# Kernel optimization log

Hardware: AMD Instinct MI355X
Metric: run time of the kernel (lower is better)

Reference implementation:

```python
import jax, jax.numpy as jnp
import numpy as np

H = 65  # LSTM units / vocab size
L = 3   # stacked layers (shared weights)

def _lstm_step(x, h, c, W, U, b):
    # Keras LSTMCell gate order: i, f, c(bar), o
    z = x @ W + h @ U + b  # [B, 4H]
    i, f, g, o = jnp.split(z, 4, axis=-1)
    i = jax.nn.sigmoid(i)
    f = jax.nn.sigmoid(f)
    g = jnp.tanh(g)
    o = jax.nn.sigmoid(o)
    c_new = f * c + i * g
    h_new = o * jnp.tanh(c_new)
    return h_new, c_new

def setup_inputs() -> dict:
    key = jax.random.key(0)
    ks = jax.random.split(key, 4)
    B, T = 50, 4096
    x = jax.random.normal(ks[0], (B, T, H), dtype=jnp.float32)
    s = 1.0 / np.sqrt(H)
    W = jax.random.normal(ks[1], (H, 4 * H), dtype=jnp.float32) * s
    U = jax.random.normal(ks[2], (H, 4 * H), dtype=jnp.float32) * s
    b = jnp.zeros((4 * H,), dtype=jnp.float32)
    Wd = jax.random.normal(ks[3], (H, H), dtype=jnp.float32) * s
    bd = jnp.zeros((H,), dtype=jnp.float32)
    return {"x": x, "W": W, "U": U, "b": b, "Wd": Wd, "bd": bd}

def reference(x, W, U, b, Wd, bd):
    B, T, _ = x.shape
    h0 = jnp.zeros((L, B, H), dtype=x.dtype)
    c0 = jnp.zeros((L, B, H), dtype=x.dtype)

    def step(carry, x_t):
        h, c = carry  # each [L, B, H]
        inp = x_t
        hs, cs = [], []
        for l in range(L):  # 3 layers, SAME weights (shared cell object)
            h_l, c_l = _lstm_step(inp, h[l], c[l], W, U, b)
            hs.append(h_l)
            cs.append(c_l)
            inp = h_l
        return (jnp.stack(hs), jnp.stack(cs)), inp  # output = top-layer hidden

    _, ys = jax.lax.scan(step, (h0, c0), jnp.swapaxes(x, 0, 1))  # ys: [T, B, H]
    ys = jnp.swapaxes(ys, 0, 1)  # [B, T, H]
    return ys @ Wd + bd
```

## Files before the change

### kernel.cpp

```cpp
#include <hip/hip_runtime.h>


#define HH    65
#define G4    260
#define TT    4096
#define NB    50
#define BLOCK 1024
#define DROWS 64

using v2f = __attribute__((ext_vector_type(2))) float;
#define PKFMA(a, b, c) __builtin_elementwise_fma((a), (b), (c))
#define KEEP(s) asm volatile("" : "+v"(s))

__device__ __forceinline__ float sigm(float x)  { return 1.0f / (1.0f + __expf(-x)); }
__device__ __forceinline__ float tanha(float x) { float e = __expf(2.0f * x); return 1.0f - 2.0f / (e + 1.0f); }

__device__ __forceinline__ float qsum8(float v) {
    int i = __float_as_int(v);
    v += __int_as_float(__builtin_amdgcn_update_dpp(0, i, 0xB1,  0xF, 0xF, true));
    i = __float_as_int(v);
    v += __int_as_float(__builtin_amdgcn_update_dpp(0, i, 0x4E,  0xF, 0xF, true));
    i = __float_as_int(v);
    v += __int_as_float(__builtin_amdgcn_update_dpp(0, i, 0x141, 0xF, 0xF, true));
    return v;
}

__global__ void __launch_bounds__(BLOCK)
__attribute__((amdgpu_waves_per_eu(4, 4)))
charrnn_rec(const float* __restrict__ x, const float* __restrict__ W,
            const float* __restrict__ U, const float* __restrict__ bv,
            float* __restrict__ out)
{
    __shared__ __align__(16) float s_hin[3][68];
    __shared__ __align__(16) float s_hrec[3][68];
    __shared__ __align__(16) float s_z[3][2][256];
    __shared__ float s_parte[3][2][4];

    const int bat  = blockIdx.x;
    const int tid  = threadIdx.x;
    const int lane = tid & 63;
    const int wv   = tid >> 6;
    const float* xb   = x   + (size_t)bat * TT * HH;
    float*       outb = out + (size_t)bat * TT * HH;

    for (int i = tid; i < 3 * 68; i += BLOCK) { (&s_hin[0][0])[i] = 0.0f; (&s_hrec[0][0])[i] = 0.0f; }

    const int w    = tid & 7;
    const int qC   = (tid >> 3) & 63;
    const int col0 = qC * 4;
    const int side = tid >> 9;
    const float* M = side ? U : W;

    v2f wa0, wa1, wa2, wa3, wb0, wb1, wb2, wb3,
        wc0, wc1, wc2, wc3, wd0, wd1, wd2, wd3;
#define WLD(v, c, q)                                                          \
    do {                                                                      \
        float t0 = M[(8 * w + 2 * (q) + 0) * G4 + col0 + (c)];                \
        float t1 = M[(8 * w + 2 * (q) + 1) * G4 + col0 + (c)];                \
        KEEP(t0); KEEP(t1);                                                   \
        v = (v2f){t0, t1};                                                    \
    } while (0)
    WLD(wa0, 0, 0); WLD(wa1, 0, 1); WLD(wa2, 0, 2); WLD(wa3, 0, 3);
    WLD(wb0, 1, 0); WLD(wb1, 1, 1); WLD(wb2, 1, 2); WLD(wb3, 1, 3);
    WLD(wc0, 2, 0); WLD(wc1, 2, 1); WLD(wc2, 2, 2); WLD(wc3, 2, 3);
    WLD(wd0, 3, 0); WLD(wd1, 3, 1); WLD(wd2, 3, 2); WLD(wd3, 3, 3);
#undef WLD
    float ws0 = (w == 7) ? M[64 * G4 + col0 + 0] : 0.0f; KEEP(ws0);
    float ws1 = (w == 7) ? M[64 * G4 + col0 + 1] : 0.0f; KEEP(ws1);
    float ws2 = (w == 7) ? M[64 * G4 + col0 + 2] : 0.0f; KEEP(ws2);
    float ws3 = (w == 7) ? M[64 * G4 + col0 + 3] : 0.0f; KEEP(ws3);

    const bool isX  = ((wv == 0) || (wv == 9)) && (lane < 32);
    const int  colX = 256 + ((lane >> 3) & 3);
    v2f e0, e1, e2, e3;
#define ELD(v, q)                                                             \
    do {                                                                      \
        float t0 = isX ? M[(8 * w + 2 * (q) + 0) * G4 + colX] : 0.0f;         \
        float t1 = isX ? M[(8 * w + 2 * (q) + 1) * G4 + colX] : 0.0f;         \
        KEEP(t0); KEEP(t1);                                                   \
        v = (v2f){t0, t1};                                                    \
    } while (0)
    ELD(e0, 0); ELD(e1, 1); ELD(e2, 2); ELD(e3, 3);
#undef ELD
    float esc = (isX && w == 7) ? M[64 * G4 + colX] : 0.0f; KEEP(esc);

    const int  cl = tid / 65, n = tid - (tid / 65) * 65;
    const bool isC = (tid < 195);
    const float bz0 = bv[n], bz1 = bv[65 + n], bz2 = bv[130 + n], bz3 = bv[195 + n];
    float creg = 0.0f;

    const bool isP  = (tid >= 959);
    const int  pidx = tid - 959;
    float cur = 0.0f, nxt = 0.0f;
    if (isP) {
        s_hin[0][pidx] = xb[pidx];
        cur = xb[HH + pidx];
    }
    __syncthreads();

    for (int r = 0; r < TT + 2; ++r) {
        if (isP) {
            const int tn = r + 2;
            nxt = (tn < TT) ? xb[(size_t)tn * HH + pidx] : 0.0f;
        }
#pragma unroll
        for (int l = 0; l < 3; ++l) {
            if ((unsigned)(r - l) < TT) {
                const float* hb = side ? &s_hrec[l][0] : &s_hin[l][0];
                const float4* h4 = (const float4*)(hb + 8 * w);
                const float4 H0 = h4[0], H1 = h4[1];
                const float  h64 = hb[64];
                const v2f hA = (v2f){H0.x, H0.y}, hB = (v2f){H0.z, H0.w};
                const v2f hC = (v2f){H1.x, H1.y}, hD = (v2f){H1.z, H1.w};
                float a0, a1, a2, a3;
#define CD(res, p0, p1, p2, p3, ps)                                           \
    {   v2f ac = hA * p0;                                                     \
        ac = PKFMA(hB, p1, ac);                                               \
        ac = PKFMA(hC, p2, ac);                                               \
        ac = PKFMA(hD, p3, ac);                                               \
        res = fmaf(h64, ps, ac.x + ac.y); }
                CD(a0, wa0, wa1, wa2, wa3, ws0)
                CD(a1, wb0, wb1, wb2, wb3, ws1)
                CD(a2, wc0, wc1, wc2, wc3, ws2)
                CD(a3, wd0, wd1, wd2, wd3, ws3)
                a0 = qsum8(a0); a1 = qsum8(a1); a2 = qsum8(a2); a3 = qsum8(a3);
                if ((lane & 7) == 0)
                    *(float4*)&s_z[l][side][col0] = make_float4(a0, a1, a2, a3);
                if (isX) {
                    float ea;
                    CD(ea, e0, e1, e2, e3, esc)
                    ea = qsum8(ea);
                    if ((lane & 7) == 0) s_parte[l][side][(lane >> 3) & 3] = ea;
                }
#undef CD
            }
        }
        __syncthreads();

        if (isC) {
            if ((unsigned)(r - cl) < TT) {
                const float zi = bz0 + s_z[cl][0][n]       + s_z[cl][1][n];
                const float zf = bz1 + s_z[cl][0][65 + n]  + s_z[cl][1][65 + n];
                const float zg = bz2 + s_z[cl][0][130 + n] + s_z[cl][1][130 + n];
                float zo;
                if (n < 61) zo = bz3 + s_z[cl][0][195 + n]    + s_z[cl][1][195 + n];
                else        zo = bz3 + s_parte[cl][0][n - 61] + s_parte[cl][1][n - 61];
                const float ig = sigm(zi), fg = sigm(zf), gg = tanha(zg), og = sigm(zo);
                creg = fmaf(fg, creg, ig * gg);
                const float h = og * tanha(creg);
                s_hrec[cl][n] = h;
                if (cl < 2) s_hin[cl + 1][n] = h;
                else        outb[(size_t)(r - cl) * HH + n] = h;
            }
        }
        if (isP) {
            if (r + 1 < TT) s_hin[0][pidx] = cur;
            cur = nxt;
        }
        __syncthreads();
    }
}

__global__ void __launch_bounds__(256, 1)
dense_head(float* __restrict__ io, const float* __restrict__ Wd, const float* __restrict__ bd)
{
    __shared__ __align__(16) float s_h[DROWS][68];
    __shared__ float s_wd[HH][HH];
    __shared__ float s_bd[HH];

    const int tid = threadIdx.x;
    float* base = io + (size_t)blockIdx.x * DROWS * HH;

    for (int i = tid; i < DROWS * HH; i += 256) {
        const int row = i / HH, k = i - row * HH;
        s_h[row][k] = base[i];
    }
    for (int i = tid; i < HH * HH; i += 256) (&s_wd[0][0])[i] = Wd[i];
    if (tid < HH) s_bd[tid] = bd[tid];
    __syncthreads();

    for (int u = tid; u < DROWS * HH; u += 256) {
        const int row = u / HH, c = u - row * HH;
        const float4* hp = (const float4*)&s_h[row][0];
        float acc = s_bd[c];
#pragma unroll
        for (int k4 = 0; k4 < 16; ++k4) {
            const float4 hv = hp[k4];
            acc = fmaf(hv.x, s_wd[4 * k4 + 0][c], acc);
            acc = fmaf(hv.y, s_wd[4 * k4 + 1][c], acc);
            acc = fmaf(hv.z, s_wd[4 * k4 + 2][c], acc);
            acc = fmaf(hv.w, s_wd[4 * k4 + 3][c], acc);
        }
        acc = fmaf(s_h[row][64], s_wd[64][c], acc);
        base[u] = acc;
    }
}

extern "C" void kernel_launch(void* const* d_in, const int* in_sizes, int n_in,
                              void* d_out, int out_size, void* d_ws, size_t ws_size,
                              hipStream_t stream)
{
    const float* x  = (const float*)d_in[0];
    const float* W  = (const float*)d_in[1];
    const float* U  = (const float*)d_in[2];
    const float* bv = (const float*)d_in[3];
    const float* Wd = (const float*)d_in[4];
    const float* bd = (const float*)d_in[5];
    float* out = (float*)d_out;

    hipLaunchKernelGGL(charrnn_rec, dim3(NB), dim3(BLOCK), 0, stream, x, W, U, bv, out);
    hipLaunchKernelGGL(dense_head, dim3(NB * TT / DROWS), dim3(256), 0, stream, out, Wd, bd);
}
```

Baseline: 6.721 ms.

## Fuse gate reduction and cell update per unit, one barrier per step

Each hidden unit is now owned by 8 lanes (4 covering W, 4 covering U). Each lane holds all four gate columns for that unit, so the DPP reduction directly produces the full gate pre-activations and the cell update runs in-lane. This drops the shared-memory z buffer and the second __syncthreads per step, and uses ping-pong buffers for h and x. In exchange, the block shrinks to 640 threads, each thread keeps twice as many weights in registers, and the activation math is computed redundantly across the 8 lanes.

```diff
diff --git a/kernel.cpp b/kernel.cpp
--- a/kernel.cpp
+++ b/kernel.cpp
@@ -5,7 +5,8 @@
 #define G4    260
 #define TT    4096
 #define NB    50
-#define BLOCK 1024
+#define BLOCK 640
+#define NMAIN 520
 #define DROWS 64
 
 using v2f = __attribute__((ext_vector_type(2))) float;
@@ -26,138 +27,125 @@
 }
 
 __global__ void __launch_bounds__(BLOCK)
-__attribute__((amdgpu_waves_per_eu(4, 4)))
+__attribute__((amdgpu_waves_per_eu(2, 3)))
 charrnn_rec(const float* __restrict__ x, const float* __restrict__ W,
             const float* __restrict__ U, const float* __restrict__ bv,
             float* __restrict__ out)
 {
-    __shared__ __align__(16) float s_hin[3][68];
-    __shared__ __align__(16) float s_hrec[3][68];
-    __shared__ __align__(16) float s_z[3][2][256];
-    __shared__ float s_parte[3][2][4];
-
-    const int bat  = blockIdx.x;
-    const int tid  = threadIdx.x;
-    const int lane = tid & 63;
-    const int wv   = tid >> 6;
+    __shared__ __align__(16) float s_h[3][2][68];
+    __shared__ __align__(16) float s_x[2][68];
+
+    const int bat = blockIdx.x, tid = threadIdx.x;
     const float* xb   = x   + (size_t)bat * TT * HH;
     float*       outb = out + (size_t)bat * TT * HH;
 
-    for (int i = tid; i < 3 * 68; i += BLOCK) { (&s_hin[0][0])[i] = 0.0f; (&s_hrec[0][0])[i] = 0.0f; }
-
-    const int w    = tid & 7;
-    const int qC   = (tid >> 3) & 63;
-    const int col0 = qC * 4;
-    const int side = tid >> 9;
-    const float* M = side ? U : W;
-
-    v2f wa0, wa1, wa2, wa3, wb0, wb1, wb2, wb3,
-        wc0, wc1, wc2, wc3, wd0, wd1, wd2, wd3;
-#define WLD(v, c, q)                                                          \
+    for (int i = tid; i < 3 * 2 * 68; i += BLOCK) (&s_h[0][0][0])[i] = 0.0f;
+
+    const bool isM  = (tid < NMAIN);
+    const int  n    = tid >> 3;
+    const int  j    = tid & 7;
+    const int  side = j >> 2;
+    const int  q    = j & 3;
+    const int  kst  = 16 * q;
+    const float* M  = side ? U : W;
+
+    v2f wA0, wA1, wA2, wA3, wA4, wA5, wA6, wA7,
+        wB0, wB1, wB2, wB3, wB4, wB5, wB6, wB7,
+        wC0, wC1, wC2, wC3, wC4, wC5, wC6, wC7,
+        wD0, wD1, wD2, wD3, wD4, wD5, wD6, wD7;
+#define WLD(v, g, pp)                                                         \
     do {                                                                      \
-        float t0 = M[(8 * w + 2 * (q) + 0) * G4 + col0 + (c)];                \
-        float t1 = M[(8 * w + 2 * (q) + 1) * G4 + col0 + (c)];                \
+        float t0 = isM ? M[(kst + 2 * (pp) + 0) * G4 + n + 65 * (g)] : 0.0f;  \
+        float t1 = isM ? M[(kst + 2 * (pp) + 1) * G4 + n + 65 * (g)] : 0.0f;  \
         KEEP(t0); KEEP(t1);                                                   \
         v = (v2f){t0, t1};                                                    \
     } while (0)
-    WLD(wa0, 0, 0); WLD(wa1, 0, 1); WLD(wa2, 0, 2); WLD(wa3, 0, 3);
-    WLD(wb0, 1, 0); WLD(wb1, 1, 1); WLD(wb2, 1, 2); WLD(wb3, 1, 3);
-    WLD(wc0, 2, 0); WLD(wc1, 2, 1); WLD(wc2, 2, 2); WLD(wc3, 2, 3);
-    WLD(wd0, 3, 0); WLD(wd1, 3, 1); WLD(wd2, 3, 2); WLD(wd3, 3, 3);
+    WLD(wA0, 0, 0); WLD(wA1, 0, 1); WLD(wA2, 0, 2); WLD(wA3, 0, 3);
+    WLD(wA4, 0, 4); WLD(wA5, 0, 5); WLD(wA6, 0, 6); WLD(wA7, 0, 7);
+    WLD(wB0, 1, 0); WLD(wB1, 1, 1); WLD(wB2, 1, 2); WLD(wB3, 1, 3);
+    WLD(wB4, 1, 4); WLD(wB5, 1, 5); WLD(wB6, 1, 6); WLD(wB7, 1, 7);
+    WLD(wC0, 2, 0); WLD(wC1, 2, 1); WLD(wC2, 2, 2); WLD(wC3, 2, 3);
+    WLD(wC4, 2, 4); WLD(wC5, 2, 5); WLD(wC6, 2, 6); WLD(wC7, 2, 7);
+    WLD(wD0, 3, 0); WLD(wD1, 3, 1); WLD(wD2, 3, 2); WLD(wD3, 3, 3);
+    WLD(wD4, 3, 4); WLD(wD5, 3, 5); WLD(wD6, 3, 6); WLD(wD7, 3, 7);
 #undef WLD
-    float ws0 = (w == 7) ? M[64 * G4 + col0 + 0] : 0.0f; KEEP(ws0);
-    float ws1 = (w == 7) ? M[64 * G4 + col0 + 1] : 0.0f; KEEP(ws1);
-    float ws2 = (w == 7) ? M[64 * G4 + col0 + 2] : 0.0f; KEEP(ws2);
-    float ws3 = (w == 7) ? M[64 * G4 + col0 + 3] : 0.0f; KEEP(ws3);
-
-    const bool isX  = ((wv == 0) || (wv == 9)) && (lane < 32);
-    const int  colX = 256 + ((lane >> 3) & 3);
-    v2f e0, e1, e2, e3;
-#define ELD(v, q)                                                             \
-    do {                                                                      \
-        float t0 = isX ? M[(8 * w + 2 * (q) + 0) * G4 + colX] : 0.0f;         \
-        float t1 = isX ? M[(8 * w + 2 * (q) + 1) * G4 + colX] : 0.0f;         \
-        KEEP(t0); KEEP(t1);                                                   \
-        v = (v2f){t0, t1};                                                    \
-    } while (0)
-    ELD(e0, 0); ELD(e1, 1); ELD(e2, 2); ELD(e3, 3);
-#undef ELD
-    float esc = (isX && w == 7) ? M[64 * G4 + colX] : 0.0f; KEEP(esc);
-
-    const int  cl = tid / 65, n = tid - (tid / 65) * 65;
-    const bool isC = (tid < 195);
-    const float bz0 = bv[n], bz1 = bv[65 + n], bz2 = bv[130 + n], bz3 = bv[195 + n];
-    float creg = 0.0f;
-
-    const bool isP  = (tid >= 959);
-    const int  pidx = tid - 959;
+    const bool hasTail = isM && (q == 3);
+    float wsA = hasTail ? M[64 * G4 + n]           : 0.0f; KEEP(wsA);
+    float wsB = hasTail ? M[64 * G4 + n + 65]      : 0.0f; KEEP(wsB);
+    float wsC = hasTail ? M[64 * G4 + n + 130]     : 0.0f; KEEP(wsC);
+    float wsD = hasTail ? M[64 * G4 + n + 195]     : 0.0f; KEEP(wsD);
+
+    const float bz0 = isM ? bv[n]       : 0.0f;
+    const float bz1 = isM ? bv[65 + n]  : 0.0f;
+    const float bz2 = isM ? bv[130 + n] : 0.0f;
+    const float bz3 = isM ? bv[195 + n] : 0.0f;
+
+    const int pidx = (tid >= 576) ? (tid - 576) : ((tid == NMAIN) ? 64 : -1);
     float cur = 0.0f, nxt = 0.0f;
-    if (isP) {
-        s_hin[0][pidx] = xb[pidx];
+    if (pidx >= 0) {
+        s_x[0][pidx] = xb[pidx];
         cur = xb[HH + pidx];
     }
+
+    float creg0 = 0.0f, creg1 = 0.0f, creg2 = 0.0f;
+    int p = 0;
     __syncthreads();
 
     for (int r = 0; r < TT + 2; ++r) {
-        if (isP) {
+        if (pidx >= 0) {
             const int tn = r + 2;
             nxt = (tn < TT) ? xb[(size_t)tn * HH + pidx] : 0.0f;
         }
+        if (isM) {
 #pragma unroll
-        for (int l = 0; l < 3; ++l) {
-            if ((unsigned)(r - l) < TT) {
-                const float* hb = side ? &s_hrec[l][0] : &s_hin[l][0];
-                const float4* h4 = (const float4*)(hb + 8 * w);
-                const float4 H0 = h4[0], H1 = h4[1];
-                const float  h64 = hb[64];
-                const v2f hA = (v2f){H0.x, H0.y}, hB = (v2f){H0.z, H0.w};
-                const v2f hC = (v2f){H1.x, H1.y}, hD = (v2f){H1.z, H1.w};
-                float a0, a1, a2, a3;
-#define CD(res, p0, p1, p2, p3, ps)                                           \
-    {   v2f ac = hA * p0;                                                     \
-        ac = PKFMA(hB, p1, ac);                                               \
-        ac = PKFMA(hC, p2, ac);                                               \
-        ac = PKFMA(hD, p3, ac);                                               \
-        res = fmaf(h64, ps, ac.x + ac.y); }
-                CD(a0, wa0, wa1, wa2, wa3, ws0)
-                CD(a1, wb0, wb1, wb2, wb3, ws1)
-                CD(a2, wc0, wc1, wc2, wc3, ws2)
-                CD(a3, wd0, wd1, wd2, wd3, ws3)
-                a0 = qsum8(a0); a1 = qsum8(a1); a2 = qsum8(a2); a3 = qsum8(a3);
-                if ((lane & 7) == 0)
-                    *(float4*)&s_z[l][side][col0] = make_float4(a0, a1, a2, a3);
-                if (isX) {
-                    float ea;
-                    CD(ea, e0, e1, e2, e3, esc)
-                    ea = qsum8(ea);
-                    if ((lane & 7) == 0) s_parte[l][side][(lane >> 3) & 3] = ea;
+            for (int l = 0; l < 3; ++l) {
+                if ((unsigned)(r - l) < TT) {
+                    const float* hb = side ? &s_h[l][p][0]
+                                           : (l == 0 ? &s_x[p][0] : &s_h[l - 1][p][0]);
+                    const float4* h4 = (const float4*)(hb + kst);
+                    const float4 H0 = h4[0], H1 = h4[1], H2 = h4[2], H3 = h4[3];
+                    const float  h64 = hb[64];
+                    const v2f hA = (v2f){H0.x, H0.y}, hB = (v2f){H0.z, H0.w},
+                              hC = (v2f){H1.x, H1.y}, hD = (v2f){H1.z, H1.w},
+                              hE = (v2f){H2.x, H2.y}, hF = (v2f){H2.z, H2.w},
+                              hG = (v2f){H3.x, H3.y}, hHv = (v2f){H3.z, H3.w};
+                    float a0, a1, a2, a3;
+#define CD(res, P0, P1, P2, P3, P4, P5, P6, P7, S)                            \
+    {   v2f ac = hA * P0;                                                     \
+        ac = PKFMA(hB, P1, ac);  ac = PKFMA(hC, P2, ac);                      \
+        ac = PKFMA(hD, P3, ac);  ac = PKFMA(hE, P4, ac);                      \
+        ac = PKFMA(hF, P5, ac);  ac = PKFMA(hG, P6, ac);                      \
+        ac = PKFMA(hHv, P7, ac);                                              \
+        res = fmaf(h64, S, ac.x + ac.y); }
+                    CD(a0, wA0, wA1, wA2, wA3, wA4, wA5, wA6, wA7, wsA)
+                    CD(a1, wB0, wB1, wB2, wB3, wB4, wB5, wB6, wB7, wsB)
+                    CD(a2, wC0, wC1, wC2, wC3, wC4, wC5, wC6, wC7, wsC)
+                    CD(a3, wD0, wD1, wD2, wD3, wD4, wD5, wD6, wD7, wsD)
+#undef CD
+                    const float z0 = qsum8(a0) + bz0;
+                    const float z1 = qsum8(a1) + bz1;
+                    const float z2 = qsum8(a2) + bz2;
+                    const float z3 = qsum8(a3) + bz3;
+                    const float ig = sigm(z0), fg = sigm(z1),
+                                gg = tanha(z2), og = sigm(z3);
+                    float c;
+                    if (l == 0)      { creg0 = fmaf(fg, creg0, ig * gg); c = creg0; }
+                    else if (l == 1) { creg1 = fmaf(fg, creg1, ig * gg); c = creg1; }
+                    else             { creg2 = fmaf(fg, creg2, ig * gg); c = creg2; }
+                    const float h = og * tanha(c);
+                    if (j == 0) {
+                        s_h[l][p ^ 1][n] = h;
+                        if (l == 2) outb[(size_t)(r - 2) * HH + n] = h;
+                    }
                 }
-#undef CD
             }
         }
+        if (pidx >= 0) {
+            if (r + 1 < TT) s_x[p ^ 1][pidx] = cur;
+            cur = nxt;
+        }
         __syncthreads();
-
-        if (isC) {
-            if ((unsigned)(r - cl) < TT) {
-                const float zi = bz0 + s_z[cl][0][n]       + s_z[cl][1][n];
-                const float zf = bz1 + s_z[cl][0][65 + n]  + s_z[cl][1][65 + n];
-                const float zg = bz2 + s_z[cl][0][130 + n] + s_z[cl][1][130 + n];
-                float zo;
-                if (n < 61) zo = bz3 + s_z[cl][0][195 + n]    + s_z[cl][1][195 + n];
-                else        zo = bz3 + s_parte[cl][0][n - 61] + s_parte[cl][1][n - 61];
-                const float ig = sigm(zi), fg = sigm(zf), gg = tanha(zg), og = sigm(zo);
-                creg = fmaf(fg, creg, ig * gg);
-                const float h = og * tanha(creg);
-                s_hrec[cl][n] = h;
-                if (cl < 2) s_hin[cl + 1][n] = h;
-                else        outb[(size_t)(r - cl) * HH + n] = h;
-            }
-        }
-        if (isP) {
-            if (r + 1 < TT) s_hin[0][pidx] = cur;
-            cur = nxt;
-        }
-        __syncthreads();
+        p ^= 1;
     }
 }
 
```

New measurement: 11.51 ms. +71.3%, slower.
